# Kernel tuning notes

Hardware: AMD Instinct MI355X
Metric: run time of the kernel (lower is better)

The kernel has to match this reference:

```python
import jax, jax.numpy as jnp
import numpy as np
from jax import lax

N, DEG, D_IN, D_FEAT, D_HID, D_REP, G = 32768, 16, 128, 256, 256, 128, 64


def setup_inputs() -> dict:
    key = jax.random.key(0)
    ks = jax.random.split(key, 24)
    def w(k, shape):
        return (jax.random.normal(k, shape, jnp.float32) / np.sqrt(shape[0])).astype(jnp.float32)
    inp = {
        "in_feat": jax.random.normal(ks[0], (N, D_IN), jnp.float32),
        "neighbors": jax.random.randint(ks[1], (N, DEG), 0, N, jnp.int32),
        "node2graph": jnp.sort(jax.random.randint(ks[2], (N,), 0, G, jnp.int32)),
        # layer 1 (SAGEConv 128 -> 256, lstm aggregator: LSTM(128,128))
        "w_ih1": w(ks[3], (4 * D_IN, D_IN)),
        "w_hh1": w(ks[4], (4 * D_IN, D_IN)),
        "b_lstm1": jnp.zeros((4 * D_IN,), jnp.float32),
        "w_self1": w(ks[5], (D_IN, D_FEAT)),
        "w_neigh1": w(ks[6], (D_IN, D_FEAT)),
        "b1": jnp.zeros((D_FEAT,), jnp.float32),
        # layer 2 (SAGEConv 256 -> 256, LSTM(256,256))
        "w_ih2": w(ks[7], (4 * D_FEAT, D_FEAT)),
        "w_hh2": w(ks[8], (4 * D_FEAT, D_FEAT)),
        "b_lstm2": jnp.zeros((4 * D_FEAT,), jnp.float32),
        "w_self2": w(ks[9], (D_FEAT, D_HID)),
        "w_neigh2": w(ks[10], (D_FEAT, D_HID)),
        "b2": jnp.zeros((D_HID,), jnp.float32),
        # heads
        "w_mu": w(ks[11], (D_HID, D_REP)),
        "b_mu": jnp.zeros((D_REP,), jnp.float32),
        "w_sigma": w(ks[12], (D_HID, D_REP)),
        "b_sigma": jnp.zeros((D_REP,), jnp.float32),
    }
    return inp


def _lstm_agg(seq, w_ih, w_hh, b):
    # seq: [N, L, D] neighbor messages; LSTM with zero init, return final hidden h.
    n, _, d = seq.shape
    h0 = jnp.zeros((n, d), seq.dtype)
    def step(carry, x):
        h, c = carry
        gates = x @ w_ih.T + h @ w_hh.T + b  # [N, 4D]
        i, f, g, o = jnp.split(gates, 4, axis=-1)  # pytorch gate order i,f,g,o
        c = jax.nn.sigmoid(f) * c + jax.nn.sigmoid(i) * jnp.tanh(g)
        h = jax.nn.sigmoid(o) * jnp.tanh(c)
        return (h, c), None
    (h, _), _ = lax.scan(step, (h0, h0), jnp.swapaxes(seq, 0, 1))
    return h


def _sage_lstm(feat, neighbors, w_ih, w_hh, b_lstm, w_self, w_neigh, b):
    msgs = feat[neighbors]                      # irregular gather [N, DEG, D]
    h_n = _lstm_agg(msgs, w_ih, w_hh, b_lstm)   # [N, D]
    return feat @ w_self + h_n @ w_neigh + b


def reference(in_feat, neighbors, node2graph,
              w_ih1, w_hh1, b_lstm1, w_self1, w_neigh1, b1,
              w_ih2, w_hh2, b_lstm2, w_self2, w_neigh2, b2,
              w_mu, b_mu, w_sigma, b_sigma):
    h = _sage_lstm(in_feat, neighbors, w_ih1, w_hh1, b_lstm1, w_self1, w_neigh1, b1)
    h = jax.nn.relu(h)
    h = _sage_lstm(h, neighbors, w_ih2, w_hh2, b_lstm2, w_self2, w_neigh2, b2)
    # dgl.mean_nodes: per-graph mean over nodes
    sums = jax.ops.segment_sum(h, node2graph, num_segments=G)
    cnts = jax.ops.segment_sum(jnp.ones((h.shape[0],), h.dtype), node2graph, num_segments=G)
    x = sums / jnp.maximum(cnts, 1.0)[:, None]
    return (x @ w_mu + b_mu, x @ w_sigma + b_sigma)
```

## Files before the change

### kernel.cpp

```cpp
#include <hip/hip_runtime.h>
#include <hip/hip_bf16.h>
#include <cstddef>

#define NN_   32768
#define DEG_  16
#define D1_   128
#define D2_   256
#define G_    64
#define DREP_ 128

typedef __attribute__((ext_vector_type(8))) short bf16x8;
typedef __attribute__((ext_vector_type(4))) float f32x4;
typedef unsigned short ushort_t;

__device__ __attribute__((aligned(16))) ushort_t g_feat1[(size_t)NN_ * D1_];
__device__ __attribute__((aligned(16))) ushort_t g_hfeat[(size_t)NN_ * D2_];
__device__ __attribute__((aligned(16))) ushort_t g_hA[(size_t)NN_ * D2_];
__device__ __attribute__((aligned(16))) ushort_t g_hB[(size_t)NN_ * D2_];
__device__ __attribute__((aligned(16))) float    g_c[(size_t)NN_ * D2_];
__device__ __attribute__((aligned(16))) float    g_P[(size_t)NN_ * 1024];
__device__ __attribute__((aligned(16))) float    g_outh[(size_t)NN_ * D2_];
__device__ __attribute__((aligned(16))) ushort_t g_wih1[512 * 128];
__device__ __attribute__((aligned(16))) ushort_t g_whh1[512 * 128];
__device__ __attribute__((aligned(16))) ushort_t g_wself1[256 * 128];
__device__ __attribute__((aligned(16))) ushort_t g_wneigh1[256 * 128];
__device__ __attribute__((aligned(16))) ushort_t g_wih2[1024 * 256];
__device__ __attribute__((aligned(16))) ushort_t g_whh2[1024 * 256];
__device__ __attribute__((aligned(16))) ushort_t g_wself2[256 * 256];
__device__ __attribute__((aligned(16))) ushort_t g_wneigh2[256 * 256];
__device__ float g_gsum[G_ * D2_];
__device__ int   g_gcnt[G_];

__device__ __forceinline__ ushort_t f2bf(float f) {
    unsigned int u = __float_as_uint(f);
    u += 0x7fffu + ((u >> 16) & 1u);
    return (ushort_t)(u >> 16);
}
__device__ __forceinline__ float sigf(float x) { return 1.f / (1.f + __expf(-x)); }
__device__ __forceinline__ float tanhf_(float x) { return 1.f - 2.f / (__expf(2.f * x) + 1.f); }

__global__ __launch_bounds__(256) void cvt_bf16(const float* __restrict__ src,
                                                ushort_t* __restrict__ dst, int n)
{
    int i = blockIdx.x * 256 + threadIdx.x;
    if (i < n) dst[i] = f2bf(src[i]);
}

__global__ __launch_bounds__(256) void cvt_bf16_T(const float* __restrict__ src,
                                                  ushort_t* __restrict__ dst, int K, int N)
{
    int i = blockIdx.x * 256 + threadIdx.x;
    if (i < K * N) {
        int k = i / N, n = i % N;
        dst[n * K + k] = f2bf(src[i]);
    }
}

template<bool DUAL, bool HAS_BIAS, bool RELU, bool OUTBF>
__global__ __launch_bounds__(256) void gemm_mfma(
    const ushort_t* __restrict__ A1, const ushort_t* __restrict__ B1,
    const ushort_t* __restrict__ A2, const ushort_t* __restrict__ B2,
    const float* __restrict__ bias, float* __restrict__ Cf,
    ushort_t* __restrict__ Cb, int M, int N, int K)
{
    __shared__ ushort_t As[64][72];
    __shared__ ushort_t Bs[64][72];
    const int tid = threadIdx.x;
    const int l = tid & 63, w = tid >> 6;
    const int m0 = blockIdx.y * 64, n0 = blockIdx.x * 64;

    f32x4 acc[4];
#pragma unroll
    for (int m = 0; m < 4; ++m) acc[m] = (f32x4){0.f, 0.f, 0.f, 0.f};

    const int npass = DUAL ? 2 : 1;
    for (int pass = 0; pass < npass; ++pass) {
        const ushort_t* __restrict__ A = (DUAL && pass) ? A2 : A1;
        const ushort_t* __restrict__ B = (DUAL && pass) ? B2 : B1;
        for (int k0 = 0; k0 < K; k0 += 64) {
#pragma unroll
            for (int i = 0; i < 2; ++i) {
                int cid = tid + 256 * i;
                int row = cid >> 3, col = (cid & 7) * 8;
                *(uint4*)&As[row][col] = *(const uint4*)&A[(size_t)(m0 + row) * K + k0 + col];
                *(uint4*)&Bs[row][col] = *(const uint4*)&B[(size_t)(n0 + row) * K + k0 + col];
            }
            __syncthreads();
#pragma unroll
            for (int kk = 0; kk < 64; kk += 32) {
                bf16x8 b = *(const bf16x8*)&Bs[16 * w + (l & 15)][kk + (l >> 4) * 8];
#pragma unroll
                for (int m = 0; m < 4; ++m) {
                    bf16x8 a = *(const bf16x8*)&As[16 * m + (l & 15)][kk + (l >> 4) * 8];
                    acc[m] = __builtin_amdgcn_mfma_f32_16x16x32_bf16(a, b, acc[m], 0, 0, 0);
                }
            }
            __syncthreads();
        }
    }

#pragma unroll
    for (int m = 0; m < 4; ++m) {
#pragma unroll
        for (int r = 0; r < 4; ++r) {
            int row = m0 + 16 * m + (l >> 4) * 4 + r;
            int col = n0 + 16 * w + (l & 15);
            float v = acc[m][r];
            if (HAS_BIAS) v += bias[col];
            if (RELU) v = fmaxf(v, 0.f);
            if (OUTBF) Cb[(size_t)row * N + col] = f2bf(v);
            else       Cf[(size_t)row * N + col] = v;
        }
    }
}

template<int D>
__global__ __launch_bounds__(256) void lstm_step(
    const ushort_t* __restrict__ h_prev, const ushort_t* __restrict__ whh,
    const float* __restrict__ P, const int* __restrict__ nbr,
    float* __restrict__ c, ushort_t* __restrict__ h_next, int t)
{
    __shared__ ushort_t As[64][72];
    __shared__ ushort_t Bs[256][72];
    const int tid = threadIdx.x;
    const int l = tid & 63, w = tid >> 6;
    const int m0 = blockIdx.x * 64;
    const int d0 = blockIdx.y * 64;

    f32x4 acc[4][4];
#pragma unroll
    for (int g = 0; g < 4; ++g)
#pragma unroll
        for (int m = 0; m < 4; ++m) acc[g][m] = (f32x4){0.f, 0.f, 0.f, 0.f};

    for (int k0 = 0; k0 < D; k0 += 64) {
#pragma unroll
        for (int i = 0; i < 2; ++i) {
            int cid = tid + 256 * i;
            int row = cid >> 3, col = (cid & 7) * 8;
            *(uint4*)&As[row][col] = *(const uint4*)&h_prev[(size_t)(m0 + row) * D + k0 + col];
        }
#pragma unroll
        for (int i = 0; i < 8; ++i) {
            int cid = tid + 256 * i;
            int row = cid >> 3, col = (cid & 7) * 8;
            int g = row >> 6, dl = row & 63;
            *(uint4*)&Bs[row][col] =
                *(const uint4*)&whh[(size_t)(g * D + d0 + dl) * D + k0 + col];
        }
        __syncthreads();
#pragma unroll
        for (int kk = 0; kk < 64; kk += 32) {
            bf16x8 a[4];
#pragma unroll
            for (int m = 0; m < 4; ++m)
                a[m] = *(const bf16x8*)&As[16 * m + (l & 15)][kk + (l >> 4) * 8];
#pragma unroll
            for (int g = 0; g < 4; ++g) {
                bf16x8 b = *(const bf16x8*)&Bs[g * 64 + 16 * w + (l & 15)][kk + (l >> 4) * 8];
#pragma unroll
                for (int m = 0; m < 4; ++m)
                    acc[g][m] = __builtin_amdgcn_mfma_f32_16x16x32_bf16(a[m], b, acc[g][m], 0, 0, 0);
            }
        }
        __syncthreads();
    }

    const int d = d0 + 16 * w + (l & 15);
#pragma unroll
    for (int m = 0; m < 4; ++m) {
#pragma unroll
        for (int r = 0; r < 4; ++r) {
            int node = m0 + 16 * m + (l >> 4) * 4 + r;
            int j = nbr[node * DEG_ + t];
            size_t base = (size_t)j * (4 * D);
            float gi = acc[0][m][r] + P[base + d];
            float gf = acc[1][m][r] + P[base + D + d];
            float gg = acc[2][m][r] + P[base + 2 * D + d];
            float go = acc[3][m][r] + P[base + 3 * D + d];
            size_t ci = (size_t)node * D + d;
            float cn = sigf(gf) * c[ci] + sigf(gi) * tanhf_(gg);
            c[ci] = cn;
            h_next[ci] = f2bf(sigf(go) * tanhf_(cn));
        }
    }
}

template<int D>
__global__ __launch_bounds__(256) void cell_first(
    const float* __restrict__ P, const int* __restrict__ nbr,
    float* __restrict__ c, ushort_t* __restrict__ h_out)
{
    int idx = blockIdx.x * 256 + threadIdx.x;
    int n = idx / D, d = idx % D;
    int j = nbr[n * DEG_];
    size_t base = (size_t)j * (4 * D);
    float gi = P[base + d];
    float gg = P[base + 2 * D + d];
    float go = P[base + 3 * D + d];
    float cn = sigf(gi) * tanhf_(gg);
    c[idx] = cn;
    h_out[idx] = f2bf(sigf(go) * tanhf_(cn));
}

__global__ void graph_counts(const int* __restrict__ n2g, int* __restrict__ cnt)
{
    __shared__ int lb[G_ + 1];
    int g = threadIdx.x;
    if (g <= G_) {
        int lo = 0, hi = NN_;
        while (lo < hi) {
            int mid = (lo + hi) >> 1;
            if (n2g[mid] < g) lo = mid + 1; else hi = mid;
        }
        lb[g] = lo;
    }
    __syncthreads();
    if (g < G_) cnt[g] = lb[g + 1] - lb[g];
}

__global__ __launch_bounds__(256) void seg_sum(
    const float* __restrict__ X, const int* __restrict__ n2g,
    float* __restrict__ gsum)
{
    int d = threadIdx.x;
    int n_start = blockIdx.x * 256;
    int cur = n2g[n_start];
    float acc = 0.f;
    for (int n = n_start; n < n_start + 256; ++n) {
        int g = n2g[n];
        if (g != cur) {
            atomicAdd(&gsum[cur * D2_ + d], acc);
            acc = 0.f;
            cur = g;
        }
        acc += X[(size_t)n * D2_ + d];
    }
    atomicAdd(&gsum[cur * D2_ + d], acc);
}

__global__ __launch_bounds__(128) void head_kernel(
    const float* __restrict__ gsum, const int* __restrict__ cnt,
    const float* __restrict__ w_mu, const float* __restrict__ b_mu,
    const float* __restrict__ w_sig, const float* __restrict__ b_sig,
    float* __restrict__ out)
{
    __shared__ float x[D2_];
    int g = blockIdx.x, j = threadIdx.x;
    float inv = 1.f / fmaxf((float)cnt[g], 1.f);
    x[j] = gsum[g * D2_ + j] * inv;
    x[j + 128] = gsum[g * D2_ + 128 + j] * inv;
    __syncthreads();
    float mu = b_mu[j], sg = b_sig[j];
    for (int k = 0; k < D2_; ++k) {
        float xv = x[k];
        mu += xv * w_mu[k * DREP_ + j];
        sg += xv * w_sig[k * DREP_ + j];
    }
    out[g * DREP_ + j] = mu;
    out[G_ * DREP_ + g * DREP_ + j] = sg;
}

extern "C" void kernel_launch(void* const* d_in, const int* in_sizes, int n_in,
                              void* d_out, int out_size, void* d_ws, size_t ws_size,
                              hipStream_t stream)
{
    const float* in_feat   = (const float*)d_in[0];
    const int*   neighbors = (const int*)d_in[1];
    const int*   node2graph= (const int*)d_in[2];
    const float* w_ih1     = (const float*)d_in[3];
    const float* w_hh1     = (const float*)d_in[4];
    const float* b_lstm1   = (const float*)d_in[5];
    const float* w_self1   = (const float*)d_in[6];
    const float* w_neigh1  = (const float*)d_in[7];
    const float* b1        = (const float*)d_in[8];
    const float* w_ih2     = (const float*)d_in[9];
    const float* w_hh2     = (const float*)d_in[10];
    const float* b_lstm2   = (const float*)d_in[11];
    const float* w_self2   = (const float*)d_in[12];
    const float* w_neigh2  = (const float*)d_in[13];
    const float* b2        = (const float*)d_in[14];
    const float* w_mu      = (const float*)d_in[15];
    const float* b_mu      = (const float*)d_in[16];
    const float* w_sigma   = (const float*)d_in[17];
    const float* b_sigma   = (const float*)d_in[18];

    void *pF1, *pHF, *pHA, *pHB, *pC, *pP, *pOH;
    void *pWI1, *pWH1, *pWS1, *pWN1, *pWI2, *pWH2, *pWS2, *pWN2, *pGS, *pGC;
    hipGetSymbolAddress(&pF1, HIP_SYMBOL(g_feat1));
    hipGetSymbolAddress(&pHF, HIP_SYMBOL(g_hfeat));
    hipGetSymbolAddress(&pHA, HIP_SYMBOL(g_hA));
    hipGetSymbolAddress(&pHB, HIP_SYMBOL(g_hB));
    hipGetSymbolAddress(&pC,  HIP_SYMBOL(g_c));
    hipGetSymbolAddress(&pP,  HIP_SYMBOL(g_P));
    hipGetSymbolAddress(&pOH, HIP_SYMBOL(g_outh));
    hipGetSymbolAddress(&pWI1, HIP_SYMBOL(g_wih1));
    hipGetSymbolAddress(&pWH1, HIP_SYMBOL(g_whh1));
    hipGetSymbolAddress(&pWS1, HIP_SYMBOL(g_wself1));
    hipGetSymbolAddress(&pWN1, HIP_SYMBOL(g_wneigh1));
    hipGetSymbolAddress(&pWI2, HIP_SYMBOL(g_wih2));
    hipGetSymbolAddress(&pWH2, HIP_SYMBOL(g_whh2));
    hipGetSymbolAddress(&pWS2, HIP_SYMBOL(g_wself2));
    hipGetSymbolAddress(&pWN2, HIP_SYMBOL(g_wneigh2));
    hipGetSymbolAddress(&pGS, HIP_SYMBOL(g_gsum));
    hipGetSymbolAddress(&pGC, HIP_SYMBOL(g_gcnt));

    ushort_t* feat1 = (ushort_t*)pF1;
    ushort_t* hfeat = (ushort_t*)pHF;
    ushort_t* hA    = (ushort_t*)pHA;
    ushort_t* hB    = (ushort_t*)pHB;
    float*    c     = (float*)pC;
    float*    P     = (float*)pP;
    float*    outh  = (float*)pOH;
    ushort_t* wih1  = (ushort_t*)pWI1;
    ushort_t* whh1  = (ushort_t*)pWH1;
    ushort_t* wself1= (ushort_t*)pWS1;
    ushort_t* wneigh1=(ushort_t*)pWN1;
    ushort_t* wih2  = (ushort_t*)pWI2;
    ushort_t* whh2  = (ushort_t*)pWH2;
    ushort_t* wself2= (ushort_t*)pWS2;
    ushort_t* wneigh2=(ushort_t*)pWN2;
    float*    gsum  = (float*)pGS;
    int*      gcnt  = (int*)pGC;

    cvt_bf16<<<(NN_ * D1_ + 255) / 256, 256, 0, stream>>>(in_feat, feat1, NN_ * D1_);
    cvt_bf16<<<(512 * 128 + 255) / 256, 256, 0, stream>>>(w_ih1, wih1, 512 * 128);
    cvt_bf16<<<(512 * 128 + 255) / 256, 256, 0, stream>>>(w_hh1, whh1, 512 * 128);
    cvt_bf16_T<<<(128 * 256 + 255) / 256, 256, 0, stream>>>(w_self1, wself1, 128, 256);
    cvt_bf16_T<<<(128 * 256 + 255) / 256, 256, 0, stream>>>(w_neigh1, wneigh1, 128, 256);
    cvt_bf16<<<(1024 * 256 + 255) / 256, 256, 0, stream>>>(w_ih2, wih2, 1024 * 256);
    cvt_bf16<<<(1024 * 256 + 255) / 256, 256, 0, stream>>>(w_hh2, whh2, 1024 * 256);
    cvt_bf16_T<<<(256 * 256 + 255) / 256, 256, 0, stream>>>(w_self2, wself2, 256, 256);
    cvt_bf16_T<<<(256 * 256 + 255) / 256, 256, 0, stream>>>(w_sigma == nullptr ? w_neigh2 : w_neigh2, wneigh2, 256, 256);

    gemm_mfma<false, true, false, false>
        <<<dim3(512 / 64, NN_ / 64), 256, 0, stream>>>(
            feat1, wih1, nullptr, nullptr, b_lstm1, P, nullptr, NN_, 512, D1_);

    cell_first<D1_><<<(NN_ * D1_) / 256, 256, 0, stream>>>(P, neighbors, c, hA);
    for (int t = 1; t < DEG_; ++t) {
        const ushort_t* hp = (t & 1) ? hA : hB;
        ushort_t*       hn = (t & 1) ? hB : hA;
        lstm_step<D1_><<<dim3(NN_ / 64, D1_ / 64), 256, 0, stream>>>(
            hp, whh1, P, neighbors, c, hn, t);
    }

    gemm_mfma<true, true, true, true>
        <<<dim3(256 / 64, NN_ / 64), 256, 0, stream>>>(
            feat1, wself1, hB, wneigh1, b1, nullptr, hfeat, NN_, D2_, D1_);

    gemm_mfma<false, true, false, false>
        <<<dim3(1024 / 64, NN_ / 64), 256, 0, stream>>>(
            hfeat, wih2, nullptr, nullptr, b_lstm2, P, nullptr, NN_, 1024, D2_);

    cell_first<D2_><<<(NN_ * D2_) / 256, 256, 0, stream>>>(P, neighbors, c, hA);
    for (int t = 1; t < DEG_; ++t) {
        const ushort_t* hp = (t & 1) ? hA : hB;
        ushort_t*       hn = (t & 1) ? hB : hA;
        lstm_step<D2_><<<dim3(NN_ / 64, D2_ / 64), 256, 0, stream>>>(
            hp, whh2, P, neighbors, c, hn, t);
    }

    gemm_mfma<true, true, false, false>
        <<<dim3(256 / 64, NN_ / 64), 256, 0, stream>>>(
            hfeat, wself2, hB, wneigh2, b2, outh, nullptr, NN_, D2_, D2_);

    hipMemsetAsync(gsum, 0, (size_t)G_ * D2_ * sizeof(float), stream);
    graph_counts<<<1, 128, 0, stream>>>(node2graph, gcnt);
    seg_sum<<<NN_ / 256, 256, 0, stream>>>(outh, node2graph, gsum);
    head_kernel<<<G_, 128, 0, stream>>>(gsum, gcnt, w_mu, b_mu, w_sigma, b_sigma,
                                        (float*)d_out);
}
```

Measured before the change: 1.814 ms.

## Store LSTM input projections in bf16 and enlarge lstm_step tiles to 128 nodes

The precomputed input-gate projections P are now written in bf16 by the GEMM and widened back to float when gathered in cell_first and lstm_step. This halves the bytes moved by the random per-neighbor gathers that dominate each recurrent step. lstm_step now uses 512 threads covering 128 nodes, so each block loads the W_hh tile once for twice as many rows. seg_sum also uses smaller node chunks to launch more blocks. The cost is bf16 rounding error in the gate preactivations, plus higher LDS and register use per block.

```diff
diff --git a/kernel.cpp b/kernel.cpp
--- a/kernel.cpp
+++ b/kernel.cpp
@@ -18,7 +18,7 @@
 __device__ __attribute__((aligned(16))) ushort_t g_hA[(size_t)NN_ * D2_];
 __device__ __attribute__((aligned(16))) ushort_t g_hB[(size_t)NN_ * D2_];
 __device__ __attribute__((aligned(16))) float    g_c[(size_t)NN_ * D2_];
-__device__ __attribute__((aligned(16))) float    g_P[(size_t)NN_ * 1024];
+__device__ __attribute__((aligned(16))) ushort_t g_P[(size_t)NN_ * 1024];
 __device__ __attribute__((aligned(16))) float    g_outh[(size_t)NN_ * D2_];
 __device__ __attribute__((aligned(16))) ushort_t g_wih1[512 * 128];
 __device__ __attribute__((aligned(16))) ushort_t g_whh1[512 * 128];
@@ -36,6 +36,9 @@
     u += 0x7fffu + ((u >> 16) & 1u);
     return (ushort_t)(u >> 16);
 }
+__device__ __forceinline__ float bf2f(ushort_t u) {
+    return __uint_as_float(((unsigned int)u) << 16);
+}
 __device__ __forceinline__ float sigf(float x) { return 1.f / (1.f + __expf(-x)); }
 __device__ __forceinline__ float tanhf_(float x) { return 1.f - 2.f / (__expf(2.f * x) + 1.f); }
 
@@ -115,16 +118,18 @@
 }
 
 template<int D>
-__global__ __launch_bounds__(256) void lstm_step(
+__global__ __launch_bounds__(512) void lstm_step(
     const ushort_t* __restrict__ h_prev, const ushort_t* __restrict__ whh,
-    const float* __restrict__ P, const int* __restrict__ nbr,
+    const ushort_t* __restrict__ P, const int* __restrict__ nbr,
     float* __restrict__ c, ushort_t* __restrict__ h_next, int t)
 {
-    __shared__ ushort_t As[64][72];
+    __shared__ ushort_t As[128][72];
     __shared__ ushort_t Bs[256][72];
     const int tid = threadIdx.x;
     const int l = tid & 63, w = tid >> 6;
-    const int m0 = blockIdx.x * 64;
+    const int mh = w >> 2;
+    const int wd = w & 3;
+    const int m0 = blockIdx.x * 128;
     const int d0 = blockIdx.y * 64;
 
     f32x4 acc[4][4];
@@ -136,13 +141,13 @@
     for (int k0 = 0; k0 < D; k0 += 64) {
 #pragma unroll
         for (int i = 0; i < 2; ++i) {
-            int cid = tid + 256 * i;
+            int cid = tid + 512 * i;
             int row = cid >> 3, col = (cid & 7) * 8;
             *(uint4*)&As[row][col] = *(const uint4*)&h_prev[(size_t)(m0 + row) * D + k0 + col];
         }
 #pragma unroll
-        for (int i = 0; i < 8; ++i) {
-            int cid = tid + 256 * i;
+        for (int i = 0; i < 4; ++i) {
+            int cid = tid + 512 * i;
             int row = cid >> 3, col = (cid & 7) * 8;
             int g = row >> 6, dl = row & 63;
             *(uint4*)&Bs[row][col] =
@@ -154,10 +159,10 @@
             bf16x8 a[4];
 #pragma unroll
             for (int m = 0; m < 4; ++m)
-                a[m] = *(const bf16x8*)&As[16 * m + (l & 15)][kk + (l >> 4) * 8];
+                a[m] = *(const bf16x8*)&As[64 * mh + 16 * m + (l & 15)][kk + (l >> 4) * 8];
 #pragma unroll
             for (int g = 0; g < 4; ++g) {
-                bf16x8 b = *(const bf16x8*)&Bs[g * 64 + 16 * w + (l & 15)][kk + (l >> 4) * 8];
+                bf16x8 b = *(const bf16x8*)&Bs[g * 64 + 16 * wd + (l & 15)][kk + (l >> 4) * 8];
 #pragma unroll
                 for (int m = 0; m < 4; ++m)
                     acc[g][m] = __builtin_amdgcn_mfma_f32_16x16x32_bf16(a[m], b, acc[g][m], 0, 0, 0);
@@ -166,18 +171,18 @@
         __syncthreads();
     }
 
-    const int d = d0 + 16 * w + (l & 15);
+    const int d = d0 + 16 * wd + (l & 15);
 #pragma unroll
     for (int m = 0; m < 4; ++m) {
 #pragma unroll
         for (int r = 0; r < 4; ++r) {
-            int node = m0 + 16 * m + (l >> 4) * 4 + r;
+            int node = m0 + 64 * mh + 16 * m + (l >> 4) * 4 + r;
             int j = nbr[node * DEG_ + t];
             size_t base = (size_t)j * (4 * D);
-            float gi = acc[0][m][r] + P[base + d];
-            float gf = acc[1][m][r] + P[base + D + d];
-            float gg = acc[2][m][r] + P[base + 2 * D + d];
-            float go = acc[3][m][r] + P[base + 3 * D + d];
+            float gi = acc[0][m][r] + bf2f(P[base + d]);
+            float gf = acc[1][m][r] + bf2f(P[base + D + d]);
+            float gg = acc[2][m][r] + bf2f(P[base + 2 * D + d]);
+            float go = acc[3][m][r] + bf2f(P[base + 3 * D + d]);
             size_t ci = (size_t)node * D + d;
             float cn = sigf(gf) * c[ci] + sigf(gi) * tanhf_(gg);
             c[ci] = cn;
@@ -188,16 +193,16 @@
 
 template<int D>
 __global__ __launch_bounds__(256) void cell_first(
-    const float* __restrict__ P, const int* __restrict__ nbr,
+    const ushort_t* __restrict__ P, const int* __restrict__ nbr,
     float* __restrict__ c, ushort_t* __restrict__ h_out)
 {
     int idx = blockIdx.x * 256 + threadIdx.x;
     int n = idx / D, d = idx % D;
     int j = nbr[n * DEG_];
     size_t base = (size_t)j * (4 * D);
-    float gi = P[base + d];
-    float gg = P[base + 2 * D + d];
-    float go = P[base + 3 * D + d];
+    float gi = bf2f(P[base + d]);
+    float gg = bf2f(P[base + 2 * D + d]);
+    float go = bf2f(P[base + 3 * D + d]);
     float cn = sigf(gi) * tanhf_(gg);
     c[idx] = cn;
     h_out[idx] = f2bf(sigf(go) * tanhf_(cn));
@@ -224,10 +229,10 @@
     float* __restrict__ gsum)
 {
     int d = threadIdx.x;
-    int n_start = blockIdx.x * 256;
+    int n_start = blockIdx.x * 64;
     int cur = n2g[n_start];
     float acc = 0.f;
-    for (int n = n_start; n < n_start + 256; ++n) {
+    for (int n = n_start; n < n_start + 64; ++n) {
         int g = n2g[n];
         if (g != cur) {
             atomicAdd(&gsum[cur * D2_ + d], acc);
@@ -310,7 +315,7 @@
     ushort_t* hA    = (ushort_t*)pHA;
     ushort_t* hB    = (ushort_t*)pHB;
     float*    c     = (float*)pC;
-    float*    P     = (float*)pP;
+    ushort_t* P     = (ushort_t*)pP;
     float*    outh  = (float*)pOH;
     ushort_t* wih1  = (ushort_t*)pWI1;
     ushort_t* whh1  = (ushort_t*)pWH1;
@@ -331,17 +336,17 @@
     cvt_bf16<<<(1024 * 256 + 255) / 256, 256, 0, stream>>>(w_ih2, wih2, 1024 * 256);
     cvt_bf16<<<(1024 * 256 + 255) / 256, 256, 0, stream>>>(w_hh2, whh2, 1024 * 256);
     cvt_bf16_T<<<(256 * 256 + 255) / 256, 256, 0, stream>>>(w_self2, wself2, 256, 256);
-    cvt_bf16_T<<<(256 * 256 + 255) / 256, 256, 0, stream>>>(w_sigma == nullptr ? w_neigh2 : w_neigh2, wneigh2, 256, 256);
-
-    gemm_mfma<false, true, false, false>
+    cvt_bf16_T<<<(256 * 256 + 255) / 256, 256, 0, stream>>>(w_neigh2, wneigh2, 256, 256);
+
+    gemm_mfma<false, true, false, true>
         <<<dim3(512 / 64, NN_ / 64), 256, 0, stream>>>(
-            feat1, wih1, nullptr, nullptr, b_lstm1, P, nullptr, NN_, 512, D1_);
+            feat1, wih1, nullptr, nullptr, b_lstm1, nullptr, P, NN_, 512, D1_);
 
     cell_first<D1_><<<(NN_ * D1_) / 256, 256, 0, stream>>>(P, neighbors, c, hA);
     for (int t = 1; t < DEG_; ++t) {
         const ushort_t* hp = (t & 1) ? hA : hB;
         ushort_t*       hn = (t & 1) ? hB : hA;
-        lstm_step<D1_><<<dim3(NN_ / 64, D1_ / 64), 256, 0, stream>>>(
+        lstm_step<D1_><<<dim3(NN_ / 128, D1_ / 64), 512, 0, stream>>>(
             hp, whh1, P, neighbors, c, hn, t);
     }
 
@@ -349,15 +354,15 @@
         <<<dim3(256 / 64, NN_ / 64), 256, 0, stream>>>(
             feat1, wself1, hB, wneigh1, b1, nullptr, hfeat, NN_, D2_, D1_);
 
-    gemm_mfma<false, true, false, false>
+    gemm_mfma<false, true, false, true>
         <<<dim3(1024 / 64, NN_ / 64), 256, 0, stream>>>(
-            hfeat, wih2, nullptr, nullptr, b_lstm2, P, nullptr, NN_, 1024, D2_);
+            hfeat, wih2, nullptr, nullptr, b_lstm2, nullptr, P, NN_, 1024, D2_);
 
     cell_first<D2_><<<(NN_ * D2_) / 256, 256, 0, stream>>>(P, neighbors, c, hA);
     for (int t = 1; t < DEG_; ++t) {
         const ushort_t* hp = (t & 1) ? hA : hB;
         ushort_t*       hn = (t & 1) ? hB : hA;
-        lstm_step<D2_><<<dim3(NN_ / 64, D2_ / 64), 256, 0, stream>>>(
+        lstm_step<D2_><<<dim3(NN_ / 128, D2_ / 64), 512, 0, stream>>>(
             hp, whh2, P, neighbors, c, hn, t);
     }
 
@@ -367,7 +372,7 @@
 
     hipMemsetAsync(gsum, 0, (size_t)G_ * D2_ * sizeof(float), stream);
     graph_counts<<<1, 128, 0, stream>>>(node2graph, gcnt);
-    seg_sum<<<NN_ / 256, 256, 0, stream>>>(outh, node2graph, gsum);
+    seg_sum<<<NN_ / 64, 256, 0, stream>>>(outh, node2graph, gsum);
     head_kernel<<<G_, 128, 0, stream>>>(gsum, gcnt, w_mu, b_mu, w_sigma, b_sigma,
                                         (float*)d_out);
 }
```

Result: slower. 1.897 ms (+4.5%).
